# Performance work log

Measured on AMD Instinct MI355X. Metric: run time of the kernel, lower is better.

## Reference

```python
import math
import jax, jax.numpy as jnp
import numpy as np

B, S, H, NH = 4, 512, 1024, 16
HD = H // NH


def setup_inputs() -> dict:
    key = jax.random.key(0)
    ks = jax.random.split(key, 16)
    scale = 1.0 / math.sqrt(H)
    inp = {
        "query": jax.random.normal(ks[0], (B, S, H), jnp.float32),
        "key": jax.random.normal(ks[1], (B, S, H), jnp.float32),
        "value": jax.random.normal(ks[2], (B, S, H), jnp.float32),
        "relation_k": jax.random.normal(ks[3], (B, S, S, HD), jnp.float32),
        "relation_v": jax.random.normal(ks[4], (B, S, S, HD), jnp.float32),
        "mask": jnp.ones((B, 1, S, S), jnp.int32),
        "Wq": jax.random.normal(ks[5], (H, H), jnp.float32) * scale,
        "bq": jnp.zeros((H,), jnp.float32),
        "Wk": jax.random.normal(ks[6], (H, H), jnp.float32) * scale,
        "bk": jnp.zeros((H,), jnp.float32),
        "Wv": jax.random.normal(ks[7], (H, H), jnp.float32) * scale,
        "bv": jnp.zeros((H,), jnp.float32),
        "Wo": jax.random.normal(ks[8], (H, H), jnp.float32) * scale,
        "bo": jnp.zeros((H,), jnp.float32),
    }
    return inp


def _split_heads(x):
    # [B,S,H] -> [B,NH,S,HD]
    return x.reshape(B, S, NH, HD).transpose(0, 2, 1, 3)


def reference(query, key, value, relation_k, relation_v, mask, Wq, bq, Wk, bk, Wv, bv, Wo, bo):
    q = _split_heads(query @ Wq.T + bq)   # [B,NH,S,HD]
    k = _split_heads(key @ Wk.T + bk)
    v = _split_heads(value @ Wv.T + bv)

    # scores: QK^T plus relation-key bias (relation shared across heads)
    qk = jnp.einsum("bhqd,bhkd->bhqk", q, k)
    qr = jnp.einsum("bhqd,bqkd->bhqk", q, relation_k)
    scores = (qk + qr) / math.sqrt(HD)
    scores = jnp.where(mask == 0, jnp.float32(-1000.0), scores)

    p = jax.nn.softmax(scores, axis=-1)   # dropout p=0 -> identity

    wv = jnp.einsum("bhqk,bhkd->bhqd", p, v)
    wr = jnp.einsum("bhqk,bqkd->bhqd", p, relation_v)
    out = (wv + wr).transpose(0, 2, 1, 3).reshape(B, S, H)
    return out @ Wo.T + bo
```

## Files before the change

kernel.cpp:

```cpp
#include <hip/hip_runtime.h>


#define NB 4
#define NS 512
#define NHID 1024
#define NHEAD 16
#define DH 64
#define SK 520

typedef short bf16x8 __attribute__((ext_vector_type(8)));
typedef float f32x4 __attribute__((ext_vector_type(4)));
typedef unsigned short u16;

__device__ __forceinline__ u16 f2bf(float f){
  unsigned u = __float_as_uint(f);
  u += 0x7FFFu + ((u >> 16) & 1u);
  return (u16)(u >> 16);
}
__device__ __forceinline__ float bf2f(u16 h){
  return __uint_as_float(((unsigned)h) << 16);
}
__device__ __forceinline__ bf16x8 packbf8(const float4& a, const float4& b){
  bf16x8 r;
  r[0]=(short)f2bf(a.x); r[1]=(short)f2bf(a.y); r[2]=(short)f2bf(a.z); r[3]=(short)f2bf(a.w);
  r[4]=(short)f2bf(b.x); r[5]=(short)f2bf(b.y); r[6]=(short)f2bf(b.z); r[7]=(short)f2bf(b.w);
  return r;
}
#define MFMA(a,b,c) __builtin_amdgcn_mfma_f32_16x16x32_bf16((a),(b),(c),0,0,0)

template<bool ABF16>
__device__ __forceinline__ void gemm_body(
    const void* A_, const float* W, const float* bias, void* out_,
    int mode, float scale, int m0, int n0, u16* lA, u16* lB){
  const int t = threadIdx.x;
  const int lane = t & 63, wid = t >> 6;
  const int wr = wid >> 1, wc = wid & 1;
  const int lr = lane & 15, kg = lane >> 4;
  f32x4 acc[4][4] = {};
  for (int k0 = 0; k0 < NHID; k0 += 32){
    if (!ABF16){
      const float* A = (const float*)A_;
      const int col = (t & 7) * 4;
      #pragma unroll
      for (int i = 0; i < 4; i++){
        const int r = (t >> 3) + 32*i;
        float4 v = *(const float4*)(A + (size_t)(m0 + r)*NHID + k0 + col);
        ushort4 pk; pk.x=f2bf(v.x); pk.y=f2bf(v.y); pk.z=f2bf(v.z); pk.w=f2bf(v.w);
        *(ushort4*)&lA[r*40 + col] = pk;
      }
    } else {
      const u16* A = (const u16*)A_;
      const int col = (t & 3) * 8;
      #pragma unroll
      for (int i = 0; i < 2; i++){
        const int r = (t >> 2) + 64*i;
        bf16x8 v = *(const bf16x8*)(A + (size_t)(m0 + r)*NHID + k0 + col);
        *(bf16x8*)&lA[r*40 + col] = v;
      }
    }
    {
      const int col = (t & 7) * 4;
      #pragma unroll
      for (int i = 0; i < 4; i++){
        const int r = (t >> 3) + 32*i;
        float4 v = *(const float4*)(W + (size_t)(n0 + r)*NHID + k0 + col);
        ushort4 pk; pk.x=f2bf(v.x); pk.y=f2bf(v.y); pk.z=f2bf(v.z); pk.w=f2bf(v.w);
        *(ushort4*)&lB[r*40 + col] = pk;
      }
    }
    __syncthreads();
    bf16x8 af[4], bfv[4];
    #pragma unroll
    for (int mt = 0; mt < 4; mt++)
      af[mt] = *(const bf16x8*)&lA[(wr*64 + mt*16 + lr)*40 + kg*8];
    #pragma unroll
    for (int nt = 0; nt < 4; nt++)
      bfv[nt] = *(const bf16x8*)&lB[(wc*64 + nt*16 + lr)*40 + kg*8];
    #pragma unroll
    for (int mt = 0; mt < 4; mt++)
      #pragma unroll
      for (int nt = 0; nt < 4; nt++)
        acc[mt][nt] = MFMA(af[mt], bfv[nt], acc[mt][nt]);
    __syncthreads();
  }
  #pragma unroll
  for (int mt = 0; mt < 4; mt++){
    const int row0 = m0 + wr*64 + mt*16 + kg*4;
    #pragma unroll
    for (int nt = 0; nt < 4; nt++){
      const int col = n0 + wc*64 + nt*16 + lr;
      const float bv = bias[col];
      float vals[4];
      #pragma unroll
      for (int r = 0; r < 4; r++) vals[r] = (acc[mt][nt][r] + bv) * scale;
      if (mode == 0){
        u16* out = (u16*)out_;
        const int h = col >> 6, d = col & 63;
        #pragma unroll
        for (int r = 0; r < 4; r++){
          const int row = row0 + r;
          const int bb = row >> 9, s = row & 511;
          out[(((size_t)(bb*NHEAD + h))*NS + s)*DH + d] = f2bf(vals[r]);
        }
      } else if (mode == 1){
        u16* out = (u16*)out_;
        const int h = col >> 6, d = col & 63;
        const int bb = row0 >> 9, s = row0 & 511;
        ushort4 pk; pk.x=f2bf(vals[0]); pk.y=f2bf(vals[1]); pk.z=f2bf(vals[2]); pk.w=f2bf(vals[3]);
        *(ushort4*)&out[(((size_t)(bb*NHEAD + h))*DH + d)*NS + s] = pk;
      } else {
        float* out = (float*)out_;
        #pragma unroll
        for (int r = 0; r < 4; r++) out[(size_t)(row0 + r)*NHID + col] = vals[r];
      }
    }
  }
}

__global__ __launch_bounds__(256, 1) void qkv_kernel(
    const float* qin, const float* kin, const float* vin,
    const float* Wq, const float* Wk, const float* Wv,
    const float* bq, const float* bk, const float* bv,
    u16* Q, u16* K, u16* Vt){
  __shared__ __align__(16) u16 lds[2*128*40];
  const int m0 = blockIdx.y*128, n0 = blockIdx.x*128;
  const int z = blockIdx.z;
  if (z == 0)      gemm_body<false>(qin, Wq, bq, Q, 0, 0.125f, m0, n0, lds, lds + 128*40);
  else if (z == 1) gemm_body<false>(kin, Wk, bk, K, 0, 1.0f,  m0, n0, lds, lds + 128*40);
  else             gemm_body<false>(vin, Wv, bv, Vt, 1, 1.0f, m0, n0, lds, lds + 128*40);
}

__global__ __launch_bounds__(256, 1) void oproj_kernel(
    const u16* A, const float* Wo, const float* bo, float* out){
  __shared__ __align__(16) u16 lds[2*128*40];
  gemm_body<true>(A, Wo, bo, out, 2, 1.0f, blockIdx.y*128, blockIdx.x*128, lds, lds + 128*40);
}

__global__ __launch_bounds__(512, 1) void attn_kernel(
    const u16* __restrict__ Q, const u16* __restrict__ K, const u16* __restrict__ Vt,
    const float* __restrict__ RK, const float* __restrict__ RV,
    u16* __restrict__ attn_out){
  __shared__ __align__(16) u16 sc[NHEAD*8*SK];
  const int b = blockIdx.y;
  const int q0 = blockIdx.x * 8;
  const int t = threadIdx.x;
  const int lane = t & 63, w = t >> 6;
  const int lr = lane & 15, kg = lane >> 4;

  #pragma unroll
  for (int ct = 0; ct < 4; ct++){
    const int kcol = w*64 + ct*16 + lr;
    for (int h = 0; h < NHEAD; h++){
      const u16* qp = Q + (((size_t)(b*NHEAD + h))*NS + q0 + (lr & 7))*DH + kg*8;
      bf16x8 a1 = *(const bf16x8*)qp;
      bf16x8 a2 = *(const bf16x8*)(qp + 32);
      const u16* kp = K + (((size_t)(b*NHEAD + h))*NS + kcol)*DH + kg*8;
      bf16x8 b1 = *(const bf16x8*)kp;
      bf16x8 b2 = *(const bf16x8*)(kp + 32);
      f32x4 d = {};
      d = MFMA(a1, b1, d);
      d = MFMA(a2, b2, d);
      #pragma unroll
      for (int r = 0; r < 4; r++){
        const int q = kg*4 + r;
        if (q < 8) sc[(h*8 + q)*SK + kcol] = f2bf(d[r]);
      }
    }
    for (int q = 0; q < 8; q++){
      const u16* qp = Q + (((size_t)(b*NHEAD + lr))*NS + q0 + q)*DH + kg*8;
      bf16x8 a1 = *(const bf16x8*)qp;
      bf16x8 a2 = *(const bf16x8*)(qp + 32);
      const float* rp = RK + (((size_t)(b*NS + q0 + q))*NS + kcol)*DH + kg*8;
      float4 f1 = *(const float4*)rp;
      float4 f2 = *(const float4*)(rp + 4);
      float4 f3 = *(const float4*)(rp + 32);
      float4 f4 = *(const float4*)(rp + 36);
      bf16x8 b1 = packbf8(f1, f2);
      bf16x8 b2 = packbf8(f3, f4);
      f32x4 d = {};
      d = MFMA(a1, b1, d);
      d = MFMA(a2, b2, d);
      #pragma unroll
      for (int r = 0; r < 4; r++){
        const int h = kg*4 + r;
        u16* p = &sc[(h*8 + q)*SK + kcol];
        *p = f2bf(bf2f(*p) + d[r]);
      }
    }
  }
  __syncthreads();

  for (int j = 0; j < 16; j++){
    const int rid = w*16 + j;
    u16* rowp = &sc[rid*SK + lane*8];
    bf16x8 v = *(const bf16x8*)rowp;
    float s0[8];
    #pragma unroll
    for (int i = 0; i < 8; i++) s0[i] = bf2f((u16)v[i]);
    float m = s0[0];
    #pragma unroll
    for (int i = 1; i < 8; i++) m = fmaxf(m, s0[i]);
    #pragma unroll
    for (int off = 32; off > 0; off >>= 1) m = fmaxf(m, __shfl_xor(m, off));
    float e[8], lsum = 0.f;
    #pragma unroll
    for (int i = 0; i < 8; i++){ e[i] = __expf(s0[i] - m); lsum += e[i]; }
    #pragma unroll
    for (int off = 32; off > 0; off >>= 1) lsum += __shfl_xor(lsum, off);
    const float inv = 1.f / lsum;
    bf16x8 o;
    #pragma unroll
    for (int i = 0; i < 8; i++) o[i] = (short)f2bf(e[i] * inv);
    *(bf16x8*)rowp = o;
  }
  __syncthreads();

  f32x4 accv[2][4] = {};
  #pragma unroll
  for (int hh = 0; hh < 2; hh++){
    const int h = w*2 + hh;
    for (int ks = 0; ks < 16; ks++){
      bf16x8 a = *(const bf16x8*)&sc[(h*8 + (lr & 7))*SK + ks*32 + kg*8];
      #pragma unroll
      for (int dt = 0; dt < 4; dt++){
        const u16* vp = Vt + (((size_t)(b*NHEAD + h))*DH + dt*16 + lr)*NS + ks*32 + kg*8;
        bf16x8 bb = *(const bf16x8*)vp;
        accv[hh][dt] = MFMA(a, bb, accv[hh][dt]);
      }
    }
  }

  f32x4 accr[4] = {};
  for (int ks = 0; ks < 16; ks++){
    bf16x8 a = *(const bf16x8*)&sc[(lr*8 + w)*SK + ks*32 + kg*8];
    #pragma unroll
    for (int dt = 0; dt < 4; dt++){
      const float* rp = RV + (((size_t)(b*NS + q0 + w))*NS + ks*32 + kg*8)*DH + dt*16 + lr;
      float4 fa, fb;
      fa.x = rp[0*DH]; fa.y = rp[1*DH]; fa.z = rp[2*DH]; fa.w = rp[3*DH];
      fb.x = rp[4*DH]; fb.y = rp[5*DH]; fb.z = rp[6*DH]; fb.w = rp[7*DH];
      bf16x8 bb = packbf8(fa, fb);
      accr[dt] = MFMA(a, bb, accr[dt]);
    }
  }
  __syncthreads();

  float* at = (float*)sc;
  #pragma unroll
  for (int hh = 0; hh < 2; hh++){
    const int h = w*2 + hh;
    #pragma unroll
    for (int dt = 0; dt < 4; dt++){
      #pragma unroll
      for (int r = 0; r < 4; r++){
        const int q = kg*4 + r;
        if (q < 8) at[q*NHID + h*64 + dt*16 + lr] = accv[hh][dt][r];
      }
    }
  }
  __syncthreads();
  #pragma unroll
  for (int dt = 0; dt < 4; dt++){
    #pragma unroll
    for (int r = 0; r < 4; r++){
      const int h = kg*4 + r;
      at[w*NHID + h*64 + dt*16 + lr] += accr[dt][r];
    }
  }
  __syncthreads();
  #pragma unroll
  for (int i = 0; i < 4; i++){
    const int c = i*256 + lane*4;
    f32x4 v4 = *(const f32x4*)&at[w*NHID + c];
    ushort4 pk; pk.x=f2bf(v4[0]); pk.y=f2bf(v4[1]); pk.z=f2bf(v4[2]); pk.w=f2bf(v4[3]);
    *(ushort4*)&attn_out[((size_t)(b*NS + q0 + w))*NHID + c] = pk;
  }
}

extern "C" void kernel_launch(void* const* d_in, const int* in_sizes, int n_in,
                              void* d_out, int out_size, void* d_ws, size_t ws_size,
                              hipStream_t stream){
  const float* qin = (const float*)d_in[0];
  const float* kin = (const float*)d_in[1];
  const float* vin = (const float*)d_in[2];
  const float* rk  = (const float*)d_in[3];
  const float* rv  = (const float*)d_in[4];
  const float* Wq = (const float*)d_in[6];
  const float* bq = (const float*)d_in[7];
  const float* Wk = (const float*)d_in[8];
  const float* bk = (const float*)d_in[9];
  const float* Wv = (const float*)d_in[10];
  const float* bv = (const float*)d_in[11];
  const float* Wo = (const float*)d_in[12];
  const float* bo = (const float*)d_in[13];

  u16* Q    = (u16*)d_ws;
  u16* K    = Q  + (size_t)2*1024*1024;
  u16* Vt   = K  + (size_t)2*1024*1024;
  u16* attn = Vt + (size_t)2*1024*1024;

  qkv_kernel<<<dim3(8, 16, 3), 256, 0, stream>>>(qin, kin, vin, Wq, Wk, Wv, bq, bk, bv, Q, K, Vt);
  attn_kernel<<<dim3(64, 4), 512, 0, stream>>>(Q, K, Vt, rk, rv, attn);
  oproj_kernel<<<dim3(8, 16), 256, 0, stream>>>(attn, Wo, bo, (float*)d_out);
}
```

Before: 286.0 us.

## Double attention block to 16 waves and repartition work per wave

Result: faster. 265.1 us (-7.3%).

```diff
diff --git a/kernel.cpp b/kernel.cpp
--- a/kernel.cpp
+++ b/kernel.cpp
@@ -136,7 +136,7 @@
   gemm_body<true>(A, Wo, bo, out, 2, 1.0f, blockIdx.y*128, blockIdx.x*128, lds, lds + 128*40);
 }
 
-__global__ __launch_bounds__(512, 1) void attn_kernel(
+__global__ __launch_bounds__(1024, 4) void attn_kernel(
     const u16* __restrict__ Q, const u16* __restrict__ K, const u16* __restrict__ Vt,
     const float* __restrict__ RK, const float* __restrict__ RV,
     u16* __restrict__ attn_out){
@@ -147,13 +147,13 @@
   const int lane = t & 63, w = t >> 6;
   const int lr = lane & 15, kg = lane >> 4;
 
-  #pragma unroll
-  for (int ct = 0; ct < 4; ct++){
-    const int kcol = w*64 + ct*16 + lr;
-    for (int h = 0; h < NHEAD; h++){
-      const u16* qp = Q + (((size_t)(b*NHEAD + h))*NS + q0 + (lr & 7))*DH + kg*8;
-      bf16x8 a1 = *(const bf16x8*)qp;
-      bf16x8 a2 = *(const bf16x8*)(qp + 32);
+  for (int h = 0; h < NHEAD; h++){
+    const u16* qp = Q + (((size_t)(b*NHEAD + h))*NS + q0 + (lr & 7))*DH + kg*8;
+    bf16x8 a1 = *(const bf16x8*)qp;
+    bf16x8 a2 = *(const bf16x8*)(qp + 32);
+    #pragma unroll
+    for (int ct = 0; ct < 2; ct++){
+      const int kcol = w*32 + ct*16 + lr;
       const u16* kp = K + (((size_t)(b*NHEAD + h))*NS + kcol)*DH + kg*8;
       bf16x8 b1 = *(const bf16x8*)kp;
       bf16x8 b2 = *(const bf16x8*)(kp + 32);
@@ -166,10 +166,14 @@
         if (q < 8) sc[(h*8 + q)*SK + kcol] = f2bf(d[r]);
       }
     }
-    for (int q = 0; q < 8; q++){
-      const u16* qp = Q + (((size_t)(b*NHEAD + lr))*NS + q0 + q)*DH + kg*8;
-      bf16x8 a1 = *(const bf16x8*)qp;
-      bf16x8 a2 = *(const bf16x8*)(qp + 32);
+  }
+  for (int q = 0; q < 8; q++){
+    const u16* qp = Q + (((size_t)(b*NHEAD + lr))*NS + q0 + q)*DH + kg*8;
+    bf16x8 a1 = *(const bf16x8*)qp;
+    bf16x8 a2 = *(const bf16x8*)(qp + 32);
+    #pragma unroll
+    for (int ct = 0; ct < 2; ct++){
+      const int kcol = w*32 + ct*16 + lr;
       const float* rp = RK + (((size_t)(b*NS + q0 + q))*NS + kcol)*DH + kg*8;
       float4 f1 = *(const float4*)rp;
       float4 f2 = *(const float4*)(rp + 4);
@@ -190,8 +194,9 @@
   }
   __syncthreads();
 
-  for (int j = 0; j < 16; j++){
-    const int rid = w*16 + j;
+  #pragma unroll
+  for (int j = 0; j < 8; j++){
+    const int rid = w*8 + j;
     u16* rowp = &sc[rid*SK + lane*8];
     bf16x8 v = *(const bf16x8*)rowp;
     float s0[8];
@@ -215,65 +220,85 @@
   }
   __syncthreads();
 
-  f32x4 accv[2][4] = {};
-  #pragma unroll
-  for (int hh = 0; hh < 2; hh++){
-    const int h = w*2 + hh;
+  f32x4 accv[4] = {};
+  {
+    const int h = w;
     for (int ks = 0; ks < 16; ks++){
       bf16x8 a = *(const bf16x8*)&sc[(h*8 + (lr & 7))*SK + ks*32 + kg*8];
       #pragma unroll
       for (int dt = 0; dt < 4; dt++){
         const u16* vp = Vt + (((size_t)(b*NHEAD + h))*DH + dt*16 + lr)*NS + ks*32 + kg*8;
         bf16x8 bb = *(const bf16x8*)vp;
-        accv[hh][dt] = MFMA(a, bb, accv[hh][dt]);
+        accv[dt] = MFMA(a, bb, accv[dt]);
       }
     }
   }
 
   f32x4 accr[4] = {};
-  for (int ks = 0; ks < 16; ks++){
-    bf16x8 a = *(const bf16x8*)&sc[(lr*8 + w)*SK + ks*32 + kg*8];
+  {
+    const int q = w >> 1, kh = w & 1;
+    for (int ks = 0; ks < 8; ks++){
+      const int kk = kh*8 + ks;
+      bf16x8 a = *(const bf16x8*)&sc[(lr*8 + q)*SK + kk*32 + kg*8];
+      #pragma unroll
+      for (int dt = 0; dt < 4; dt++){
+        const float* rp = RV + (((size_t)(b*NS + q0 + q))*NS + kk*32 + kg*8)*DH + dt*16 + lr;
+        float4 fa, fb;
+        fa.x = rp[0*DH]; fa.y = rp[1*DH]; fa.z = rp[2*DH]; fa.w = rp[3*DH];
+        fb.x = rp[4*DH]; fb.y = rp[5*DH]; fb.z = rp[6*DH]; fb.w = rp[7*DH];
+        bf16x8 bb = packbf8(fa, fb);
+        accr[dt] = MFMA(a, bb, accr[dt]);
+      }
+    }
+  }
+  __syncthreads();
+
+  float* at = (float*)sc;
+  {
+    const int h = w;
     #pragma unroll
     for (int dt = 0; dt < 4; dt++){
-      const float* rp = RV + (((size_t)(b*NS + q0 + w))*NS + ks*32 + kg*8)*DH + dt*16 + lr;
-      float4 fa, fb;
-      fa.x = rp[0*DH]; fa.y = rp[1*DH]; fa.z = rp[2*DH]; fa.w = rp[3*DH];
-      fb.x = rp[4*DH]; fb.y = rp[5*DH]; fb.z = rp[6*DH]; fb.w = rp[7*DH];
-      bf16x8 bb = packbf8(fa, fb);
-      accr[dt] = MFMA(a, bb, accr[dt]);
-    }
-  }
-  __syncthreads();
-
-  float* at = (float*)sc;
-  #pragma unroll
-  for (int hh = 0; hh < 2; hh++){
-    const int h = w*2 + hh;
+      #pragma unroll
+      for (int r = 0; r < 4; r++){
+        const int q = kg*4 + r;
+        if (q < 8) at[q*NHID + h*64 + dt*16 + lr] = accv[dt][r];
+      }
+    }
+  }
+  __syncthreads();
+  if ((w & 1) == 0){
+    const int q = w >> 1;
     #pragma unroll
     for (int dt = 0; dt < 4; dt++){
       #pragma unroll
       for (int r = 0; r < 4; r++){
-        const int q = kg*4 + r;
-        if (q < 8) at[q*NHID + h*64 + dt*16 + lr] = accv[hh][dt][r];
-      }
-    }
-  }
-  __syncthreads();
-  #pragma unroll
-  for (int dt = 0; dt < 4; dt++){
-    #pragma unroll
-    for (int r = 0; r < 4; r++){
-      const int h = kg*4 + r;
-      at[w*NHID + h*64 + dt*16 + lr] += accr[dt][r];
-    }
-  }
-  __syncthreads();
-  #pragma unroll
-  for (int i = 0; i < 4; i++){
-    const int c = i*256 + lane*4;
-    f32x4 v4 = *(const f32x4*)&at[w*NHID + c];
-    ushort4 pk; pk.x=f2bf(v4[0]); pk.y=f2bf(v4[1]); pk.z=f2bf(v4[2]); pk.w=f2bf(v4[3]);
-    *(ushort4*)&attn_out[((size_t)(b*NS + q0 + w))*NHID + c] = pk;
+        const int h = kg*4 + r;
+        at[q*NHID + h*64 + dt*16 + lr] += accr[dt][r];
+      }
+    }
+  }
+  __syncthreads();
+  if ((w & 1) == 1){
+    const int q = w >> 1;
+    #pragma unroll
+    for (int dt = 0; dt < 4; dt++){
+      #pragma unroll
+      for (int r = 0; r < 4; r++){
+        const int h = kg*4 + r;
+        at[q*NHID + h*64 + dt*16 + lr] += accr[dt][r];
+      }
+    }
+  }
+  __syncthreads();
+  {
+    const int q = w >> 1;
+    #pragma unroll
+    for (int i = 0; i < 2; i++){
+      const int c = (w & 1)*512 + i*256 + lane*4;
+      f32x4 v4 = *(const f32x4*)&at[q*NHID + c];
+      ushort4 pk; pk.x=f2bf(v4[0]); pk.y=f2bf(v4[1]); pk.z=f2bf(v4[2]); pk.w=f2bf(v4[3]);
+      *(ushort4*)&attn_out[((size_t)(b*NS + q0 + q))*NHID + c] = pk;
+    }
   }
 }
 
@@ -300,6 +325,6 @@
   u16* attn = Vt + (size_t)2*1024*1024;
 
   qkv_kernel<<<dim3(8, 16, 3), 256, 0, stream>>>(qin, kin, vin, Wq, Wk, Wv, bq, bk, bv, Q, K, Vt);
-  attn_kernel<<<dim3(64, 4), 512, 0, stream>>>(Q, K, Vt, rk, rv, attn);
+  attn_kernel<<<dim3(64, 4), 1024, 0, stream>>>(Q, K, Vt, rk, rv, attn);
   oproj_kernel<<<dim3(8, 16), 256, 0, stream>>>(attn, Wo, bo, (float*)d_out);
 }
```

## Split fused attention kernel into scores, softmax, wv and wr kernels

Applied to the files above, without the earlier changes.

Measured after the change: 300.4 us. +5.0%, slower.

```diff
diff --git a/kernel.cpp b/kernel.cpp
--- a/kernel.cpp
+++ b/kernel.cpp
@@ -6,7 +6,7 @@
 #define NHID 1024
 #define NHEAD 16
 #define DH 64
-#define SK 520
+#define RS 144
 
 typedef short bf16x8 __attribute__((ext_vector_type(8)));
 typedef float f32x4 __attribute__((ext_vector_type(4)));
@@ -136,25 +136,25 @@
   gemm_body<true>(A, Wo, bo, out, 2, 1.0f, blockIdx.y*128, blockIdx.x*128, lds, lds + 128*40);
 }
 
-__global__ __launch_bounds__(512, 1) void attn_kernel(
-    const u16* __restrict__ Q, const u16* __restrict__ K, const u16* __restrict__ Vt,
-    const float* __restrict__ RK, const float* __restrict__ RV,
-    u16* __restrict__ attn_out){
-  __shared__ __align__(16) u16 sc[NHEAD*8*SK];
+__global__ __launch_bounds__(256, 4) void scores_kernel(
+    const u16* __restrict__ Q, const u16* __restrict__ K,
+    const float* __restrict__ RK, u16* __restrict__ SC){
+  __shared__ __align__(16) u16 tile[NHEAD*8*RS];
   const int b = blockIdx.y;
-  const int q0 = blockIdx.x * 8;
-  const int t = threadIdx.x;
-  const int lane = t & 63, w = t >> 6;
+  const int qt = blockIdx.x >> 2, kt = blockIdx.x & 3;
+  const int q0 = qt*8, k0 = kt*128;
+  const int t = threadIdx.x, lane = t & 63, w = t >> 6;
   const int lr = lane & 15, kg = lane >> 4;
 
-  #pragma unroll
-  for (int ct = 0; ct < 4; ct++){
-    const int kcol = w*64 + ct*16 + lr;
-    for (int h = 0; h < NHEAD; h++){
-      const u16* qp = Q + (((size_t)(b*NHEAD + h))*NS + q0 + (lr & 7))*DH + kg*8;
-      bf16x8 a1 = *(const bf16x8*)qp;
-      bf16x8 a2 = *(const bf16x8*)(qp + 32);
-      const u16* kp = K + (((size_t)(b*NHEAD + h))*NS + kcol)*DH + kg*8;
+  #pragma unroll 2
+  for (int h = 0; h < NHEAD; h++){
+    const u16* qp = Q + ((size_t)(b*NHEAD + h)*NS + q0 + (lr & 7))*DH + kg*8;
+    bf16x8 a1 = *(const bf16x8*)qp;
+    bf16x8 a2 = *(const bf16x8*)(qp + 32);
+    #pragma unroll
+    for (int ct = 0; ct < 2; ct++){
+      const int kl = w*32 + ct*16 + lr;
+      const u16* kp = K + ((size_t)(b*NHEAD + h)*NS + k0 + kl)*DH + kg*8;
       bf16x8 b1 = *(const bf16x8*)kp;
       bf16x8 b2 = *(const bf16x8*)(kp + 32);
       f32x4 d = {};
@@ -163,14 +163,19 @@
       #pragma unroll
       for (int r = 0; r < 4; r++){
         const int q = kg*4 + r;
-        if (q < 8) sc[(h*8 + q)*SK + kcol] = f2bf(d[r]);
-      }
-    }
-    for (int q = 0; q < 8; q++){
-      const u16* qp = Q + (((size_t)(b*NHEAD + lr))*NS + q0 + q)*DH + kg*8;
-      bf16x8 a1 = *(const bf16x8*)qp;
-      bf16x8 a2 = *(const bf16x8*)(qp + 32);
-      const float* rp = RK + (((size_t)(b*NS + q0 + q))*NS + kcol)*DH + kg*8;
+        if (q < 8) tile[(h*8 + q)*RS + kl] = f2bf(d[r]);
+      }
+    }
+  }
+  #pragma unroll 2
+  for (int q = 0; q < 8; q++){
+    const u16* qp = Q + ((size_t)(b*NHEAD + lr)*NS + q0 + q)*DH + kg*8;
+    bf16x8 a1 = *(const bf16x8*)qp;
+    bf16x8 a2 = *(const bf16x8*)(qp + 32);
+    #pragma unroll
+    for (int ct = 0; ct < 2; ct++){
+      const int kl = w*32 + ct*16 + lr;
+      const float* rp = RK + ((size_t)(b*NS + q0 + q)*NS + k0 + kl)*DH + kg*8;
       float4 f1 = *(const float4*)rp;
       float4 f2 = *(const float4*)(rp + 4);
       float4 f3 = *(const float4*)(rp + 32);
@@ -182,98 +187,96 @@
       d = MFMA(a2, b2, d);
       #pragma unroll
       for (int r = 0; r < 4; r++){
-        const int h = kg*4 + r;
-        u16* p = &sc[(h*8 + q)*SK + kcol];
+        u16* p = &tile[((kg*4 + r)*8 + q)*RS + kl];
         *p = f2bf(bf2f(*p) + d[r]);
       }
     }
   }
   __syncthreads();
-
-  for (int j = 0; j < 16; j++){
-    const int rid = w*16 + j;
-    u16* rowp = &sc[rid*SK + lane*8];
-    bf16x8 v = *(const bf16x8*)rowp;
+  #pragma unroll
+  for (int i = 0; i < 8; i++){
+    const int f = t*8 + i*2048;
+    const int h = f >> 10, q = (f >> 7) & 7, kl = f & 127;
+    bf16x8 v = *(const bf16x8*)&tile[(h*8 + q)*RS + kl];
+    *(bf16x8*)&SC[((size_t)(b*NHEAD + h)*NS + q0 + q)*NS + k0 + kl] = v;
+  }
+}
+
+__global__ __launch_bounds__(256, 4) void softmax_kernel(u16* SC){
+  const int t = threadIdx.x, lane = t & 63, w = t >> 6;
+  #pragma unroll
+  for (int i = 0; i < 4; i++){
+    const size_t row = (size_t)blockIdx.x*16 + w*4 + i;
+    u16* rp = SC + row*NS + lane*8;
+    bf16x8 v = *(const bf16x8*)rp;
     float s0[8];
     #pragma unroll
-    for (int i = 0; i < 8; i++) s0[i] = bf2f((u16)v[i]);
+    for (int j = 0; j < 8; j++) s0[j] = bf2f((u16)v[j]);
     float m = s0[0];
     #pragma unroll
-    for (int i = 1; i < 8; i++) m = fmaxf(m, s0[i]);
+    for (int j = 1; j < 8; j++) m = fmaxf(m, s0[j]);
     #pragma unroll
     for (int off = 32; off > 0; off >>= 1) m = fmaxf(m, __shfl_xor(m, off));
     float e[8], lsum = 0.f;
     #pragma unroll
-    for (int i = 0; i < 8; i++){ e[i] = __expf(s0[i] - m); lsum += e[i]; }
+    for (int j = 0; j < 8; j++){ e[j] = __expf(s0[j] - m); lsum += e[j]; }
     #pragma unroll
     for (int off = 32; off > 0; off >>= 1) lsum += __shfl_xor(lsum, off);
     const float inv = 1.f / lsum;
     bf16x8 o;
     #pragma unroll
-    for (int i = 0; i < 8; i++) o[i] = (short)f2bf(e[i] * inv);
-    *(bf16x8*)rowp = o;
-  }
-  __syncthreads();
-
-  f32x4 accv[2][4] = {};
-  #pragma unroll
-  for (int hh = 0; hh < 2; hh++){
-    const int h = w*2 + hh;
-    for (int ks = 0; ks < 16; ks++){
-      bf16x8 a = *(const bf16x8*)&sc[(h*8 + (lr & 7))*SK + ks*32 + kg*8];
-      #pragma unroll
-      for (int dt = 0; dt < 4; dt++){
-        const u16* vp = Vt + (((size_t)(b*NHEAD + h))*DH + dt*16 + lr)*NS + ks*32 + kg*8;
-        bf16x8 bb = *(const bf16x8*)vp;
-        accv[hh][dt] = MFMA(a, bb, accv[hh][dt]);
-      }
-    }
-  }
-
-  f32x4 accr[4] = {};
+    for (int j = 0; j < 8; j++) o[j] = (short)f2bf(e[j] * inv);
+    *(bf16x8*)rp = o;
+  }
+}
+
+__global__ __launch_bounds__(256, 4) void wv_kernel(
+    const u16* __restrict__ SC, const u16* __restrict__ Vt, float* __restrict__ WV){
+  const int b = blockIdx.y;
+  const int h = blockIdx.x >> 3, qt = blockIdx.x & 7;
+  const int t = threadIdx.x, lane = t & 63, w = t >> 6;
+  const int lr = lane & 15, kg = lane >> 4;
+  const int q0 = qt*64 + w*16;
+  f32x4 acc[4] = {};
+  #pragma unroll 2
   for (int ks = 0; ks < 16; ks++){
-    bf16x8 a = *(const bf16x8*)&sc[(lr*8 + w)*SK + ks*32 + kg*8];
+    bf16x8 a = *(const bf16x8*)&SC[((size_t)(b*NHEAD + h)*NS + q0 + lr)*NS + ks*32 + kg*8];
     #pragma unroll
     for (int dt = 0; dt < 4; dt++){
-      const float* rp = RV + (((size_t)(b*NS + q0 + w))*NS + ks*32 + kg*8)*DH + dt*16 + lr;
-      float4 fa, fb;
-      fa.x = rp[0*DH]; fa.y = rp[1*DH]; fa.z = rp[2*DH]; fa.w = rp[3*DH];
-      fb.x = rp[4*DH]; fb.y = rp[5*DH]; fb.z = rp[6*DH]; fb.w = rp[7*DH];
-      bf16x8 bb = packbf8(fa, fb);
-      accr[dt] = MFMA(a, bb, accr[dt]);
-    }
-  }
-  __syncthreads();
-
-  float* at = (float*)sc;
-  #pragma unroll
-  for (int hh = 0; hh < 2; hh++){
-    const int h = w*2 + hh;
-    #pragma unroll
-    for (int dt = 0; dt < 4; dt++){
-      #pragma unroll
-      for (int r = 0; r < 4; r++){
-        const int q = kg*4 + r;
-        if (q < 8) at[q*NHID + h*64 + dt*16 + lr] = accv[hh][dt][r];
-      }
-    }
-  }
-  __syncthreads();
-  #pragma unroll
-  for (int dt = 0; dt < 4; dt++){
-    #pragma unroll
-    for (int r = 0; r < 4; r++){
-      const int h = kg*4 + r;
-      at[w*NHID + h*64 + dt*16 + lr] += accr[dt][r];
-    }
-  }
-  __syncthreads();
-  #pragma unroll
-  for (int i = 0; i < 4; i++){
-    const int c = i*256 + lane*4;
-    f32x4 v4 = *(const f32x4*)&at[w*NHID + c];
-    ushort4 pk; pk.x=f2bf(v4[0]); pk.y=f2bf(v4[1]); pk.z=f2bf(v4[2]); pk.w=f2bf(v4[3]);
-    *(ushort4*)&attn_out[((size_t)(b*NS + q0 + w))*NHID + c] = pk;
+      const u16* vp = Vt + ((size_t)(b*NHEAD + h)*DH + dt*16 + lr)*NS + ks*32 + kg*8;
+      bf16x8 bb = *(const bf16x8*)vp;
+      acc[dt] = MFMA(a, bb, acc[dt]);
+    }
+  }
+  #pragma unroll
+  for (int dt = 0; dt < 4; dt++)
+    #pragma unroll
+    for (int r = 0; r < 4; r++)
+      WV[((size_t)(b*NS) + q0 + kg*4 + r)*NHID + h*64 + dt*16 + lr] = acc[dt][r];
+}
+
+__global__ __launch_bounds__(256, 4) void wr_kernel(
+    const u16* __restrict__ SC, const float* __restrict__ RV,
+    const float* __restrict__ WV, u16* __restrict__ AT){
+  const int b = blockIdx.y, q = blockIdx.x;
+  const int t = threadIdx.x, lane = t & 63, w = t >> 6;
+  const int lr = lane & 15, kg = lane >> 4;
+  f32x4 acc = {};
+  #pragma unroll 2
+  for (int kk = 0; kk < 16; kk++){
+    bf16x8 a = *(const bf16x8*)&SC[((size_t)(b*NHEAD + lr)*NS + q)*NS + kk*32 + kg*8];
+    const float* rp = RV + ((size_t)(b*NS + q)*NS + kk*32 + kg*8)*DH + w*16 + lr;
+    float4 fa, fb;
+    fa.x = rp[0*DH]; fa.y = rp[1*DH]; fa.z = rp[2*DH]; fa.w = rp[3*DH];
+    fb.x = rp[4*DH]; fb.y = rp[5*DH]; fb.z = rp[6*DH]; fb.w = rp[7*DH];
+    bf16x8 bb = packbf8(fa, fb);
+    acc = MFMA(a, bb, acc);
+  }
+  #pragma unroll
+  for (int r = 0; r < 4; r++){
+    const int c = (kg*4 + r)*64 + w*16 + lr;
+    const size_t o = ((size_t)(b*NS) + q)*NHID + c;
+    AT[o] = f2bf(WV[o] + acc[r]);
   }
 }
 
@@ -294,12 +297,18 @@
   const float* Wo = (const float*)d_in[12];
   const float* bo = (const float*)d_in[13];
 
-  u16* Q    = (u16*)d_ws;
-  u16* K    = Q  + (size_t)2*1024*1024;
-  u16* Vt   = K  + (size_t)2*1024*1024;
-  u16* attn = Vt + (size_t)2*1024*1024;
+  char* ws = (char*)d_ws;
+  u16*   Q  = (u16*)(ws);
+  u16*   K  = (u16*)(ws + (size_t)4*1024*1024);
+  u16*   Vt = (u16*)(ws + (size_t)8*1024*1024);
+  u16*   AT = (u16*)(ws + (size_t)12*1024*1024);
+  float* WV = (float*)(ws + (size_t)16*1024*1024);
+  u16*   SC = (u16*)(ws + (size_t)24*1024*1024);
 
   qkv_kernel<<<dim3(8, 16, 3), 256, 0, stream>>>(qin, kin, vin, Wq, Wk, Wv, bq, bk, bv, Q, K, Vt);
-  attn_kernel<<<dim3(64, 4), 512, 0, stream>>>(Q, K, Vt, rk, rv, attn);
-  oproj_kernel<<<dim3(8, 16), 256, 0, stream>>>(attn, Wo, bo, (float*)d_out);
-}
+  scores_kernel<<<dim3(256, 4), 256, 0, stream>>>(Q, K, rk, SC);
+  softmax_kernel<<<2048, 256, 0, stream>>>(SC);
+  wv_kernel<<<dim3(128, 4), 256, 0, stream>>>(SC, Vt, WV);
+  wr_kernel<<<dim3(512, 4), 256, 0, stream>>>(SC, rv, WV, AT);
+  oproj_kernel<<<dim3(8, 16), 256, 0, stream>>>(AT, Wo, bo, (float*)d_out);
+}
```
